# Optimization experiments

Hardware: AMD Instinct MI355X
Metric: run time of the kernel (lower is better)

Reference implementation:

```python
import jax, jax.numpy as jnp
import numpy as np

K = 3          # pooling factor (init k)
H_OUT = 8      # number of bilinear heads
H_DIM = 512    # hidden dim after pooling
BN_EPS = 1e-5
NEG_INF = -jnp.inf


def setup_inputs() -> dict:
    key = jax.random.key(0)
    ks = jax.random.split(key, 8)
    b, vn, qn, vd, qd = 16, 256, 256, 512, 768
    hk = H_DIM * K
    return {
        "v": jax.random.normal(ks[0], (b, vn, vd), jnp.float32),
        "q": jax.random.normal(ks[1], (b, qn, qd), jnp.float32),
        "Wv": jax.random.normal(ks[2], (hk, vd), jnp.float32) * 0.05,
        "bv": jax.random.normal(ks[3], (hk,), jnp.float32) * 0.05,
        "Wq": jax.random.normal(ks[4], (hk, qd), jnp.float32) * 0.05,
        "bq": jax.random.normal(ks[5], (hk,), jnp.float32) * 0.05,
        "h_mat": jax.random.normal(ks[6], (1, H_OUT, 1, hk), jnp.float32),
        "h_bias": jax.random.normal(ks[7], (1, H_OUT, 1, 1), jnp.float32),
        "bn_gamma": jnp.ones((H_DIM,), jnp.float32),
        "bn_beta": jnp.zeros((H_DIM,), jnp.float32),
    }


def _forward(v, q, Wv, bv, Wq, bq, h_mat, h_bias, bn_gamma, bn_beta):
    # FCNet (eval mode: dropout is identity; weight_norm folded into W)
    v_ = jax.nn.relu(jnp.einsum("bvd,kd->bvk", v, Wv) + bv)   # [b, vn, h_dim*k]
    q_ = jax.nn.relu(jnp.einsum("bqd,kd->bqk", q, Wq) + bq)   # [b, qn, h_dim*k]

    # Bilinear attention maps: [b, h_out, vn, qn]
    att = jnp.einsum("xhyk,bvk,bqk->bhvq", h_mat, v_, q_) + h_bias

    # v_mask / q_mask (all-zero token rows masked to -inf)
    v_zero = jnp.sum(jnp.abs(v), axis=2) == 0                  # [b, vn]
    q_zero = jnp.sum(jnp.abs(q), axis=2) == 0                  # [b, qn]
    att = jnp.where(v_zero[:, None, :, None], NEG_INF, att)
    att = jnp.where(q_zero[:, None, None, :], NEG_INF, att)

    # Fused per-head attention pooling, summed over heads (original Python loop)
    fused = jnp.einsum("bhvq,bqk->bhvk", att, q_)
    logits_k = jnp.einsum("bvk,bhvk->bk", v_, fused)           # [b, h_dim*k]

    # AvgPool1d(k, stride=k) * k  == sum over groups of k
    b = logits_k.shape[0]
    logits = logits_k.reshape(b, H_DIM, K).sum(axis=2)         # [b, h_dim]

    # BatchNorm1d (training-mode batch statistics, biased variance)
    mu = logits.mean(axis=0)
    var = logits.var(axis=0)
    logits = (logits - mu) * jax.lax.rsqrt(var + BN_EPS) * bn_gamma + bn_beta
    return logits, att


def reference(v, q, Wv, bv, Wq, bq, h_mat, h_bias, bn_gamma, bn_beta):
    return _forward(v, q, Wv, bv, Wq, bq, h_mat, h_bias, bn_gamma, bn_beta)
```

## Files before the change

### kernel.cpp

```cpp
#include <hip/hip_runtime.h>
#include <math.h>

#define BB    16
#define VN    256
#define QN    256
#define VD    512
#define QD    768
#define HK    1536
#define HDIM  512

typedef _Float16 half8 __attribute__((ext_vector_type(8)));
typedef _Float16 half4 __attribute__((ext_vector_type(4)));
typedef float f32x4 __attribute__((ext_vector_type(4)));

__global__ __launch_bounds__(256) void conv_mask2(
    const float* __restrict__ v, const float* __restrict__ q,
    _Float16* __restrict__ v16, _Float16* __restrict__ q16,
    float* __restrict__ vz, float* __restrict__ qz) {
    int which = blockIdx.y;
    const float* src = which ? q : v;
    _Float16* dst = which ? q16 : v16;
    float* outz = which ? qz : vz;
    int D = which ? QD : VD;
    int w = threadIdx.x >> 6, ln = threadIdx.x & 63;
    int row = blockIdx.x * 4 + w;
    const float* p = src + (size_t)row * D;
    _Float16* d = dst + (size_t)row * D;
    float s = 0.f;
    for (int c = ln * 4; c < D; c += 256) {
        float4 x = *(const float4*)(p + c);
        s += fabsf(x.x) + fabsf(x.y) + fabsf(x.z) + fabsf(x.w);
        half4 hh = {(_Float16)x.x, (_Float16)x.y, (_Float16)x.z, (_Float16)x.w};
        *(half4*)(d + c) = hh;
    }
    for (int off = 32; off > 0; off >>= 1) s += __shfl_down(s, off);
    if (ln == 0) outz[row] = (s == 0.f) ? 1.f : 0.f;
}

__global__ __launch_bounds__(256) void conv_w3(
    const float* __restrict__ Wv, _Float16* __restrict__ Wv16, int n4v,
    const float* __restrict__ Wq, _Float16* __restrict__ Wq16, int n4q,
    const float* __restrict__ hm, _Float16* __restrict__ hs16) {
    if (blockIdx.y == 2) {
        int k = blockIdx.x * 256 + threadIdx.x;
        if (k >= HK) return;
        float s = 0.f;
#pragma unroll
        for (int h = 0; h < 8; ++h) {
            float x = hm[h * HK + k];
            s += x;
            hs16[h * HK + k] = (_Float16)x;
        }
        hs16[8 * HK + k] = (_Float16)s;
        return;
    }
    const float* src = blockIdx.y ? Wq : Wv;
    _Float16* dst = blockIdx.y ? Wq16 : Wv16;
    int n4 = blockIdx.y ? n4q : n4v;
    int i = blockIdx.x * 256 + threadIdx.x;
    if (i < n4) {
        float4 x = ((const float4*)src)[i];
        half4 h = {(_Float16)x.x, (_Float16)x.y, (_Float16)x.z, (_Float16)x.w};
        ((half4*)dst)[i] = h;
    }
}

__global__ __launch_bounds__(128) void proj_lds(
    const _Float16* __restrict__ Ain, const _Float16* __restrict__ W16,
    const float* __restrict__ bias, _Float16* __restrict__ C16, int K) {
    __shared__ _Float16 As[64 * 64];
    __shared__ _Float16 Bs[64 * 64];
    int m0 = blockIdx.y * 64, n0 = blockIdx.x * 64;
    int t = threadIdx.x;
    int w = t >> 6, ln = t & 63, quad = ln >> 4, r16 = ln & 15;
    int arow = t >> 3, aseg = t & 7;
    int sg = aseg ^ (arow & 7);
    const _Float16* ApG = Ain + (size_t)(m0 + arow) * K + aseg * 8;
    const _Float16* BpG = W16 + (size_t)(n0 + arow) * K + aseg * 8;
    half8 ra[4], rb[4];
#pragma unroll
    for (int c = 0; c < 4; ++c) {
        ra[c] = *(const half8*)(ApG + (size_t)c * 16 * K);
        rb[c] = *(const half8*)(BpG + (size_t)c * 16 * K);
    }
    f32x4 acc[2][4] = {};
    for (int k0 = 0; k0 < K; k0 += 64) {
        __syncthreads();
#pragma unroll
        for (int c = 0; c < 4; ++c) {
            *(half8*)&As[(c * 16 + arow) * 64 + sg * 8] = ra[c];
            *(half8*)&Bs[(c * 16 + arow) * 64 + sg * 8] = rb[c];
        }
        __syncthreads();
        if (k0 + 64 < K) {
#pragma unroll
            for (int c = 0; c < 4; ++c) {
                ra[c] = *(const half8*)(ApG + (size_t)c * 16 * K + k0 + 64);
                rb[c] = *(const half8*)(BpG + (size_t)c * 16 * K + k0 + 64);
            }
        }
#pragma unroll
        for (int kc = 0; kc < 2; ++kc) {
            half8 af[2], bf[4];
#pragma unroll
            for (int fi = 0; fi < 2; ++fi) {
                int rl = w * 32 + fi * 16 + r16;
                af[fi] = *(const half8*)&As[rl * 64 + ((kc * 4 + quad) ^ (rl & 7)) * 8];
            }
#pragma unroll
            for (int fj = 0; fj < 4; ++fj) {
                int rl = fj * 16 + r16;
                bf[fj] = *(const half8*)&Bs[rl * 64 + ((kc * 4 + quad) ^ (rl & 7)) * 8];
            }
#pragma unroll
            for (int fi = 0; fi < 2; ++fi)
#pragma unroll
                for (int fj = 0; fj < 4; ++fj)
                    acc[fi][fj] = __builtin_amdgcn_mfma_f32_16x16x32_f16(
                        af[fi], bf[fj], acc[fi][fj], 0, 0, 0);
        }
    }
#pragma unroll
    for (int fi = 0; fi < 2; ++fi) {
#pragma unroll
        for (int r = 0; r < 4; ++r) {
            int m = m0 + w * 32 + fi * 16 + quad * 4 + r;
#pragma unroll
            for (int fj = 0; fj < 4; ++fj) {
                int n = n0 + fj * 16 + r16;
                float x = acc[fi][fj][r] + bias[n];
                C16[(size_t)m * HK + n] = (_Float16)fmaxf(x, 0.f);
            }
        }
    }
}

__global__ __launch_bounds__(256, 2) void att42(
    const _Float16* __restrict__ v16, const _Float16* __restrict__ q16,
    const _Float16* __restrict__ hs16, const float* __restrict__ hb,
    const float* __restrict__ vz, const float* __restrict__ qz,
    float* __restrict__ att_out, _Float16* __restrict__ A16) {
    __shared__ _Float16 As[64 * 64];
    __shared__ _Float16 Bs[32 * 64];
    __shared__ _Float16 Hl[8 * HK];
    int b = blockIdx.z;
    int i0 = blockIdx.y * 64, j0 = blockIdx.x * 32;
    int t = threadIdx.x;
    int w = t >> 6, ln = t & 63, quad = ln >> 4, r16 = ln & 15;
    int iw = w & 1, hg = w >> 1, h0 = hg * 4;
    int arow = t >> 2, as0 = t & 3;
    int brow = t >> 3, bs0 = t & 7;
    for (int u = t * 8; u < 8 * HK; u += 256 * 8)
        *(half8*)&Hl[u] = *(const half8*)(hs16 + u);
    const _Float16* ApG = v16 + (size_t)b * VN * HK + (size_t)(i0 + arow) * HK;
    const _Float16* BpG = q16 + (size_t)b * QN * HK + (size_t)(j0 + brow) * HK;
    half8 ra[2], rb;
    ra[0] = *(const half8*)(ApG + as0 * 8);
    ra[1] = *(const half8*)(ApG + as0 * 8 + 32);
    rb    = *(const half8*)(BpG + bs0 * 8);
    f32x4 acc[4][2][2] = {};
    for (int it = 0; it < 24; ++it) {
        __syncthreads();
        *(half8*)&As[arow * 64 + ((as0    ) ^ (arow & 7)) * 8] = ra[0];
        *(half8*)&As[arow * 64 + ((as0 + 4) ^ (arow & 7)) * 8] = ra[1];
        *(half8*)&Bs[brow * 64 + ((bs0    ) ^ (brow & 7)) * 8] = rb;
        __syncthreads();
        if (it + 1 < 24) {
            int kn = (it + 1) * 64;
            ra[0] = *(const half8*)(ApG + kn + as0 * 8);
            ra[1] = *(const half8*)(ApG + kn + as0 * 8 + 32);
            rb    = *(const half8*)(BpG + kn + bs0 * 8);
        }
        int kb = it * 64;
#pragma unroll
        for (int kc = 0; kc < 2; ++kc) {
            half8 af[2], bf[2];
#pragma unroll
            for (int fi = 0; fi < 2; ++fi) {
                int rl = iw * 32 + fi * 16 + r16;
                af[fi] = *(const half8*)&As[rl * 64 + ((kc * 4 + quad) ^ (rl & 7)) * 8];
            }
#pragma unroll
            for (int fj = 0; fj < 2; ++fj) {
                int rl = fj * 16 + r16;
                bf[fj] = *(const half8*)&Bs[rl * 64 + ((kc * 4 + quad) ^ (rl & 7)) * 8];
            }
#pragma unroll
            for (int hh = 0; hh < 4; ++hh) {
                half8 hmv = *(const half8*)&Hl[(h0 + hh) * HK + kb + (kc * 4 + quad) * 8];
#pragma unroll
                for (int fi = 0; fi < 2; ++fi) {
                    half8 am = af[fi] * hmv;
#pragma unroll
                    for (int fj = 0; fj < 2; ++fj)
                        acc[hh][fi][fj] = __builtin_amdgcn_mfma_f32_16x16x32_f16(
                            am, bf[fj], acc[hh][fi][fj], 0, 0, 0);
                }
            }
        }
    }
    float s[2][2][4];
#pragma unroll
    for (int fi = 0; fi < 2; ++fi)
#pragma unroll
        for (int fj = 0; fj < 2; ++fj)
#pragma unroll
            for (int r = 0; r < 4; ++r) {
                float ss = 0.f;
#pragma unroll
                for (int hh = 0; hh < 4; ++hh) ss += acc[hh][fi][fj][r];
                s[fi][fj][r] = ss;
            }
    float hbv[4];
#pragma unroll
    for (int hh = 0; hh < 4; ++hh) hbv[hh] = hb[h0 + hh];
    float hbsum = 0.f;
#pragma unroll
    for (int h = 0; h < 8; ++h) hbsum += hb[h];
    float qm[2];
#pragma unroll
    for (int fj = 0; fj < 2; ++fj) qm[fj] = qz[b * QN + j0 + fj * 16 + r16];
    float* outb = att_out + (size_t)b * 8 * VN * QN;
#pragma unroll
    for (int fi = 0; fi < 2; ++fi) {
#pragma unroll
        for (int r = 0; r < 4; ++r) {
            int i = i0 + iw * 32 + fi * 16 + quad * 4 + r;
            float vm = vz[b * VN + i];
#pragma unroll
            for (int fj = 0; fj < 2; ++fj) {
                int j = j0 + fj * 16 + r16;
                bool msk = (vm != 0.f) || (qm[fj] != 0.f);
#pragma unroll
                for (int hh = 0; hh < 4; ++hh) {
                    float x = acc[hh][fi][fj][r] + hbv[hh];
                    if (msk) x = -INFINITY;
                    outb[(size_t)(h0 + hh) * VN * QN + (size_t)i * QN + j] = x;
                }
            }
        }
    }
    __syncthreads();
    float* Red = (float*)As;
    if (hg) {
#pragma unroll
        for (int fi = 0; fi < 2; ++fi)
#pragma unroll
            for (int fj = 0; fj < 2; ++fj)
#pragma unroll
                for (int r = 0; r < 4; ++r)
                    Red[iw * 1024 + (fi * 16 + quad * 4 + r) * 32 + fj * 16 + r16] =
                        s[fi][fj][r];
    }
    __syncthreads();
    if (!hg) {
        _Float16* Ab = A16 + (size_t)b * VN * QN;
#pragma unroll
        for (int fi = 0; fi < 2; ++fi) {
#pragma unroll
            for (int r = 0; r < 4; ++r) {
                int i = i0 + iw * 32 + fi * 16 + quad * 4 + r;
                float vm = vz[b * VN + i];
#pragma unroll
                for (int fj = 0; fj < 2; ++fj) {
                    int j = j0 + fj * 16 + r16;
                    float tot = s[fi][fj][r] +
                                Red[iw * 1024 + (fi * 16 + quad * 4 + r) * 32 + fj * 16 + r16] +
                                hbsum;
                    if (vm != 0.f || qm[fj] != 0.f) tot = -INFINITY;
                    Ab[(size_t)i * QN + j] = (_Float16)tot;
                }
            }
        }
    }
}

__global__ __launch_bounds__(256) void transpose_q16(const _Float16* __restrict__ q16,
                                                     _Float16* __restrict__ q16t) {
    __shared__ _Float16 Ls[32][72];
    int b = blockIdx.z;
    int k0 = blockIdx.x * 64, j0 = blockIdx.y * 32;
    int t = threadIdx.x;
    const _Float16* src = q16 + (size_t)b * QN * HK;
    int tj = t >> 3, tk = (t & 7) * 8;
    half8 vv = *(const half8*)(src + (size_t)(j0 + tj) * HK + k0 + tk);
#pragma unroll
    for (int e = 0; e < 8; ++e) Ls[tj][tk + e] = vv[e];
    __syncthreads();
    int ok = t >> 2, oj = (t & 3) * 8;
    half8 ov;
#pragma unroll
    for (int e = 0; e < 8; ++e) ov[e] = Ls[oj + e][ok];
    *(half8*)(q16t + (size_t)b * HK * QN + (size_t)(k0 + ok) * QN + j0 + oj) = ov;
}

__global__ __launch_bounds__(256) void t_lk_mfma(
    const _Float16* __restrict__ A16, const _Float16* __restrict__ q16t,
    const _Float16* __restrict__ v16, float* __restrict__ lk) {
    __shared__ _Float16 As[256 * 32];
    __shared__ _Float16 Bs[64 * 32];
    __shared__ float red[16][64];
    int b = blockIdx.y;
    int k0 = blockIdx.x * 64;
    int t = threadIdx.x;
    int w = t >> 6, ln = t & 63, quad = ln >> 4, r16 = ln & 15;
    const _Float16* Ab = A16 + (size_t)b * VN * QN;
    const _Float16* Qt = q16t + (size_t)b * HK * QN + (size_t)k0 * QN;
    int ar = t >> 2, aseg = t & 3;
    f32x4 acc[4][4] = {};
    for (int j0 = 0; j0 < QN; j0 += 32) {
        half8 a0 = *(const half8*)(Ab + (size_t)(ar +   0) * QN + j0 + aseg * 8);
        half8 a1 = *(const half8*)(Ab + (size_t)(ar +  64) * QN + j0 + aseg * 8);
        half8 a2 = *(const half8*)(Ab + (size_t)(ar + 128) * QN + j0 + aseg * 8);
        half8 a3 = *(const half8*)(Ab + (size_t)(ar + 192) * QN + j0 + aseg * 8);
        half8 bv = *(const half8*)(Qt + (size_t)ar * QN + j0 + aseg * 8);
        __syncthreads();
        *(half8*)&As[(ar +   0) * 32 + aseg * 8] = a0;
        *(half8*)&As[(ar +  64) * 32 + aseg * 8] = a1;
        *(half8*)&As[(ar + 128) * 32 + aseg * 8] = a2;
        *(half8*)&As[(ar + 192) * 32 + aseg * 8] = a3;
        *(half8*)&Bs[ar * 32 + aseg * 8] = bv;
        __syncthreads();
        half8 af[4], bf[4];
#pragma unroll
        for (int fi = 0; fi < 4; ++fi)
            af[fi] = *(const half8*)&As[(w * 64 + fi * 16 + r16) * 32 + quad * 8];
#pragma unroll
        for (int fj = 0; fj < 4; ++fj)
            bf[fj] = *(const half8*)&Bs[(fj * 16 + r16) * 32 + quad * 8];
#pragma unroll
        for (int fi = 0; fi < 4; ++fi)
#pragma unroll
            for (int fj = 0; fj < 4; ++fj)
                acc[fi][fj] = __builtin_amdgcn_mfma_f32_16x16x32_f16(
                    af[fi], bf[fj], acc[fi][fj], 0, 0, 0);
    }
    const _Float16* Vb = v16 + (size_t)b * VN * HK;
    float part[4] = {0.f, 0.f, 0.f, 0.f};
#pragma unroll
    for (int fi = 0; fi < 4; ++fi) {
#pragma unroll
        for (int r = 0; r < 4; ++r) {
            int i = w * 64 + fi * 16 + quad * 4 + r;
#pragma unroll
            for (int fj = 0; fj < 4; ++fj) {
                float vv = (float)Vb[(size_t)i * HK + k0 + fj * 16 + r16];
                part[fj] += acc[fi][fj][r] * vv;
            }
        }
    }
#pragma unroll
    for (int fj = 0; fj < 4; ++fj)
        red[w * 4 + quad][fj * 16 + r16] = part[fj];
    __syncthreads();
    if (t < 64) {
        float s = 0.f;
#pragma unroll
        for (int g = 0; g < 16; ++g) s += red[g][t];
        lk[b * HK + k0 + t] = s;
    }
}

__global__ __launch_bounds__(256) void bn_kernel(
    const float* __restrict__ lk, const float* __restrict__ gamma,
    const float* __restrict__ beta, float* __restrict__ out) {
    int d = blockIdx.x * blockDim.x + threadIdx.x;
    if (d >= HDIM) return;
    float l[BB];
    float mu = 0.f;
#pragma unroll
    for (int b = 0; b < BB; ++b) {
        const float* p = lk + b * HK + 3 * d;
        float s = p[0] + p[1] + p[2];
        l[b] = s;
        mu += s;
    }
    mu *= (1.f / BB);
    float var = 0.f;
#pragma unroll
    for (int b = 0; b < BB; ++b) {
        float dd = l[b] - mu;
        var += dd * dd;
    }
    var *= (1.f / BB);
    float inv = rsqrtf(var + 1e-5f);
    float g = gamma[d], be = beta[d];
#pragma unroll
    for (int b = 0; b < BB; ++b)
        out[b * HDIM + d] = (l[b] - mu) * inv * g + be;
}

extern "C" void kernel_launch(void* const* d_in, const int* in_sizes, int n_in,
                              void* d_out, int out_size, void* d_ws, size_t ws_size,
                              hipStream_t stream) {
    const float* v  = (const float*)d_in[0];
    const float* q  = (const float*)d_in[1];
    const float* Wv = (const float*)d_in[2];
    const float* bv = (const float*)d_in[3];
    const float* Wq = (const float*)d_in[4];
    const float* bq = (const float*)d_in[5];
    const float* hm = (const float*)d_in[6];
    const float* hb = (const float*)d_in[7];
    const float* gamma = (const float*)d_in[8];
    const float* beta  = (const float*)d_in[9];

    float* out_logits = (float*)d_out;
    float* out_att    = out_logits + BB * HDIM;

    _Float16* h = (_Float16*)d_ws;
    _Float16* v16   = h;
    _Float16* q16   = v16 + (size_t)BB * VN * HK;
    _Float16* q16t  = q16 + (size_t)BB * QN * HK;
    _Float16* A16   = q16t + (size_t)BB * HK * QN;
    _Float16* v16in = A16 + (size_t)BB * VN * QN;
    _Float16* q16in = v16in + (size_t)BB * VN * VD;
    _Float16* Wv16  = q16in + (size_t)BB * QN * QD;
    _Float16* Wq16  = Wv16 + (size_t)HK * VD;
    _Float16* hs16  = Wq16 + (size_t)HK * QD;
    float* lk = (float*)(hs16 + 9 * HK + 8);
    float* vz = lk + BB * HK;
    float* qz = vz + BB * VN;

    conv_mask2<<<dim3(BB * VN / 4, 2), 256, 0, stream>>>(v, q, v16in, q16in, vz, qz);
    conv_w3<<<dim3((HK * QD / 4 + 255) / 256, 3), 256, 0, stream>>>(
        Wv, Wv16, HK * VD / 4, Wq, Wq16, HK * QD / 4, hm, hs16);

    proj_lds<<<dim3(HK / 64, BB * VN / 64), 128, 0, stream>>>(v16in, Wv16, bv, v16, VD);
    proj_lds<<<dim3(HK / 64, BB * QN / 64), 128, 0, stream>>>(q16in, Wq16, bq, q16, QD);

    att42<<<dim3(QN / 32, VN / 64, BB), 256, 0, stream>>>(
        v16, q16, hs16, hb, vz, qz, out_att, A16);

    transpose_q16<<<dim3(HK / 64, QN / 32, BB), 256, 0, stream>>>(q16, q16t);

    t_lk_mfma<<<dim3(HK / 64, BB), 256, 0, stream>>>(A16, q16t, v16, lk);

    bn_kernel<<<dim3((HDIM + 255) / 256), 256, 0, stream>>>(lk, gamma, beta, out_logits);
}
```

Before: 195.2 us.

## Double-buffer LDS tiles in attention kernel and swizzle block order

The attention-map kernel now keeps two LDS buffers for the v and q tiles and prefetches two K-steps ahead, so each iteration needs one barrier instead of two and global loads overlap with MFMA work. Global load mapping changes to 8 threads per row with full 64-element row segments. The grid becomes 1D with a swizzle that spreads consecutive blocks across batches and tiles, aimed at better L2/XCD locality. LDS use rises by one extra 6 KB tile set, which could affect occupancy at 2 blocks per CU.

```diff
diff --git a/kernel.cpp b/kernel.cpp
--- a/kernel.cpp
+++ b/kernel.cpp
@@ -135,41 +135,54 @@
     }
 }
 
-__global__ __launch_bounds__(256, 2) void att42(
+__global__ __launch_bounds__(256, 2) void att_db(
     const _Float16* __restrict__ v16, const _Float16* __restrict__ q16,
     const _Float16* __restrict__ hs16, const float* __restrict__ hb,
     const float* __restrict__ vz, const float* __restrict__ qz,
     float* __restrict__ att_out, _Float16* __restrict__ A16) {
-    __shared__ _Float16 As[64 * 64];
-    __shared__ _Float16 Bs[32 * 64];
+    __shared__ _Float16 As[2][64 * 64];
+    __shared__ _Float16 Bs[2][32 * 64];
     __shared__ _Float16 Hl[8 * HK];
-    int b = blockIdx.z;
-    int i0 = blockIdx.y * 64, j0 = blockIdx.x * 32;
+    int lin = blockIdx.x;
+    int swz = ((lin & 7) << 6) | (lin >> 3);
+    int jb = swz & 7, ib = (swz >> 3) & 3, b = swz >> 5;
+    int i0 = ib * 64, j0 = jb * 32;
     int t = threadIdx.x;
     int w = t >> 6, ln = t & 63, quad = ln >> 4, r16 = ln & 15;
     int iw = w & 1, hg = w >> 1, h0 = hg * 4;
-    int arow = t >> 2, as0 = t & 3;
-    int brow = t >> 3, bs0 = t & 7;
+    int arow = t >> 3, aseg = t & 7;
+    int sg = (aseg ^ (arow & 7)) * 8;
     for (int u = t * 8; u < 8 * HK; u += 256 * 8)
         *(half8*)&Hl[u] = *(const half8*)(hs16 + u);
-    const _Float16* ApG = v16 + (size_t)b * VN * HK + (size_t)(i0 + arow) * HK;
-    const _Float16* BpG = q16 + (size_t)b * QN * HK + (size_t)(j0 + brow) * HK;
+    const _Float16* ApG = v16 + (size_t)b * VN * HK + (size_t)(i0 + arow) * HK + aseg * 8;
+    const _Float16* BpG = q16 + (size_t)b * QN * HK + (size_t)(j0 + arow) * HK + aseg * 8;
     half8 ra[2], rb;
-    ra[0] = *(const half8*)(ApG + as0 * 8);
-    ra[1] = *(const half8*)(ApG + as0 * 8 + 32);
-    rb    = *(const half8*)(BpG + bs0 * 8);
+    ra[0] = *(const half8*)(ApG);
+    ra[1] = *(const half8*)(ApG + (size_t)32 * HK);
+    rb    = *(const half8*)(BpG);
+    *(half8*)&As[0][arow * 64 + sg] = ra[0];
+    *(half8*)&As[0][(arow + 32) * 64 + sg] = ra[1];
+    *(half8*)&Bs[0][arow * 64 + sg] = rb;
+    ra[0] = *(const half8*)(ApG + 64);
+    ra[1] = *(const half8*)(ApG + (size_t)32 * HK + 64);
+    rb    = *(const half8*)(BpG + 64);
     f32x4 acc[4][2][2] = {};
     for (int it = 0; it < 24; ++it) {
         __syncthreads();
-        *(half8*)&As[arow * 64 + ((as0    ) ^ (arow & 7)) * 8] = ra[0];
-        *(half8*)&As[arow * 64 + ((as0 + 4) ^ (arow & 7)) * 8] = ra[1];
-        *(half8*)&Bs[brow * 64 + ((bs0    ) ^ (brow & 7)) * 8] = rb;
-        __syncthreads();
+        int cur = it & 1;
+        const _Float16* Ac = As[cur];
+        const _Float16* Bc = Bs[cur];
         if (it + 1 < 24) {
-            int kn = (it + 1) * 64;
-            ra[0] = *(const half8*)(ApG + kn + as0 * 8);
-            ra[1] = *(const half8*)(ApG + kn + as0 * 8 + 32);
-            rb    = *(const half8*)(BpG + kn + bs0 * 8);
+            int nxt = cur ^ 1;
+            *(half8*)&As[nxt][arow * 64 + sg] = ra[0];
+            *(half8*)&As[nxt][(arow + 32) * 64 + sg] = ra[1];
+            *(half8*)&Bs[nxt][arow * 64 + sg] = rb;
+        }
+        if (it + 2 < 24) {
+            int kn = (it + 2) * 64;
+            ra[0] = *(const half8*)(ApG + kn);
+            ra[1] = *(const half8*)(ApG + (size_t)32 * HK + kn);
+            rb    = *(const half8*)(BpG + kn);
         }
         int kb = it * 64;
 #pragma unroll
@@ -178,12 +191,12 @@
 #pragma unroll
             for (int fi = 0; fi < 2; ++fi) {
                 int rl = iw * 32 + fi * 16 + r16;
-                af[fi] = *(const half8*)&As[rl * 64 + ((kc * 4 + quad) ^ (rl & 7)) * 8];
+                af[fi] = *(const half8*)&Ac[rl * 64 + ((kc * 4 + quad) ^ (rl & 7)) * 8];
             }
 #pragma unroll
             for (int fj = 0; fj < 2; ++fj) {
                 int rl = fj * 16 + r16;
-                bf[fj] = *(const half8*)&Bs[rl * 64 + ((kc * 4 + quad) ^ (rl & 7)) * 8];
+                bf[fj] = *(const half8*)&Bc[rl * 64 + ((kc * 4 + quad) ^ (rl & 7)) * 8];
             }
 #pragma unroll
             for (int hh = 0; hh < 4; ++hh) {
@@ -241,7 +254,7 @@
         }
     }
     __syncthreads();
-    float* Red = (float*)As;
+    float* Red = (float*)&As[0][0];
     if (hg) {
 #pragma unroll
         for (int fi = 0; fi < 2; ++fi)
@@ -428,7 +441,7 @@
     proj_lds<<<dim3(HK / 64, BB * VN / 64), 128, 0, stream>>>(v16in, Wv16, bv, v16, VD);
     proj_lds<<<dim3(HK / 64, BB * QN / 64), 128, 0, stream>>>(q16in, Wq16, bq, q16, QD);
 
-    att42<<<dim3(QN / 32, VN / 64, BB), 256, 0, stream>>>(
+    att_db<<<dim3(512), 256, 0, stream>>>(
         v16, q16, hs16, hb, vz, qz, out_att, A16);
 
     transpose_q16<<<dim3(HK / 64, QN / 32, BB), 256, 0, stream>>>(q16, q16t);
```

New measurement: 189.6 us. -2.9%, faster.

## Replace LDS-staged attention kernel with direct global-load MFMA kernel and swizzled grid

Applied to the files above, without the earlier changes.

Rewrites the bilinear attention kernel so each wave loads its A, B and h_mat fragments straight from global memory (relying on L1/L2), dropping the shared-memory staging, the per-iteration barriers and the 24KB h_mat LDS copy. Blocks shrink to 128 threads covering a 32x32 tile with two head groups, launched as a flat 1D grid with a swizzle that places neighbouring tiles on different blocks. It aims to cut LDS traffic and synchronisation and raise occupancy. The cost is redundant global/cache loads, since v and q rows are no longer shared across waves, and smaller tiles mean more total fragment reads.

```diff
diff --git a/kernel.cpp b/kernel.cpp
--- a/kernel.cpp
+++ b/kernel.cpp
@@ -135,62 +135,43 @@
     }
 }
 
-__global__ __launch_bounds__(256, 2) void att42(
+__global__ __launch_bounds__(128, 3) void att_nolds(
     const _Float16* __restrict__ v16, const _Float16* __restrict__ q16,
     const _Float16* __restrict__ hs16, const float* __restrict__ hb,
     const float* __restrict__ vz, const float* __restrict__ qz,
     float* __restrict__ att_out, _Float16* __restrict__ A16) {
-    __shared__ _Float16 As[64 * 64];
-    __shared__ _Float16 Bs[32 * 64];
-    __shared__ _Float16 Hl[8 * HK];
-    int b = blockIdx.z;
-    int i0 = blockIdx.y * 64, j0 = blockIdx.x * 32;
+    __shared__ float Red[32 * 32];
+    int lin = blockIdx.x;
+    int swz = ((lin & 7) << 7) | (lin >> 3);
+    int jb = swz & 7, ib = (swz >> 3) & 7, b = swz >> 6;
+    int i0 = ib * 32, j0 = jb * 32;
     int t = threadIdx.x;
-    int w = t >> 6, ln = t & 63, quad = ln >> 4, r16 = ln & 15;
-    int iw = w & 1, hg = w >> 1, h0 = hg * 4;
-    int arow = t >> 2, as0 = t & 3;
-    int brow = t >> 3, bs0 = t & 7;
-    for (int u = t * 8; u < 8 * HK; u += 256 * 8)
-        *(half8*)&Hl[u] = *(const half8*)(hs16 + u);
-    const _Float16* ApG = v16 + (size_t)b * VN * HK + (size_t)(i0 + arow) * HK;
-    const _Float16* BpG = q16 + (size_t)b * QN * HK + (size_t)(j0 + brow) * HK;
-    half8 ra[2], rb;
-    ra[0] = *(const half8*)(ApG + as0 * 8);
-    ra[1] = *(const half8*)(ApG + as0 * 8 + 32);
-    rb    = *(const half8*)(BpG + bs0 * 8);
+    int hg = t >> 6, ln = t & 63, quad = ln >> 4, r16 = ln & 15;
+    int h0 = hg * 4;
+    const _Float16* Av = v16 + (size_t)b * VN * HK + (size_t)(i0 + r16) * HK + quad * 8;
+    const _Float16* Bq = q16 + (size_t)b * QN * HK + (size_t)(j0 + r16) * HK + quad * 8;
+    const _Float16* Hm = hs16 + (size_t)h0 * HK + quad * 8;
     f32x4 acc[4][2][2] = {};
     for (int it = 0; it < 24; ++it) {
-        __syncthreads();
-        *(half8*)&As[arow * 64 + ((as0    ) ^ (arow & 7)) * 8] = ra[0];
-        *(half8*)&As[arow * 64 + ((as0 + 4) ^ (arow & 7)) * 8] = ra[1];
-        *(half8*)&Bs[brow * 64 + ((bs0    ) ^ (brow & 7)) * 8] = rb;
-        __syncthreads();
-        if (it + 1 < 24) {
-            int kn = (it + 1) * 64;
-            ra[0] = *(const half8*)(ApG + kn + as0 * 8);
-            ra[1] = *(const half8*)(ApG + kn + as0 * 8 + 32);
-            rb    = *(const half8*)(BpG + kn + bs0 * 8);
-        }
         int kb = it * 64;
 #pragma unroll
         for (int kc = 0; kc < 2; ++kc) {
-            half8 af[2], bf[2];
-#pragma unroll
-            for (int fi = 0; fi < 2; ++fi) {
-                int rl = iw * 32 + fi * 16 + r16;
-                af[fi] = *(const half8*)&As[rl * 64 + ((kc * 4 + quad) ^ (rl & 7)) * 8];
-            }
-#pragma unroll
-            for (int fj = 0; fj < 2; ++fj) {
-                int rl = fj * 16 + r16;
-                bf[fj] = *(const half8*)&Bs[rl * 64 + ((kc * 4 + quad) ^ (rl & 7)) * 8];
-            }
+            int ko = kb + kc * 32;
+            half8 af[2], bf[2], hmv[4];
+#pragma unroll
+            for (int fi = 0; fi < 2; ++fi)
+                af[fi] = *(const half8*)(Av + (size_t)fi * 16 * HK + ko);
+#pragma unroll
+            for (int fj = 0; fj < 2; ++fj)
+                bf[fj] = *(const half8*)(Bq + (size_t)fj * 16 * HK + ko);
+#pragma unroll
+            for (int hh = 0; hh < 4; ++hh)
+                hmv[hh] = *(const half8*)(Hm + (size_t)hh * HK + ko);
 #pragma unroll
             for (int hh = 0; hh < 4; ++hh) {
-                half8 hmv = *(const half8*)&Hl[(h0 + hh) * HK + kb + (kc * 4 + quad) * 8];
 #pragma unroll
                 for (int fi = 0; fi < 2; ++fi) {
-                    half8 am = af[fi] * hmv;
+                    half8 am = af[fi] * hmv[hh];
 #pragma unroll
                     for (int fj = 0; fj < 2; ++fj)
                         acc[hh][fi][fj] = __builtin_amdgcn_mfma_f32_16x16x32_f16(
@@ -225,7 +206,7 @@
     for (int fi = 0; fi < 2; ++fi) {
 #pragma unroll
         for (int r = 0; r < 4; ++r) {
-            int i = i0 + iw * 32 + fi * 16 + quad * 4 + r;
+            int i = i0 + fi * 16 + quad * 4 + r;
             float vm = vz[b * VN + i];
 #pragma unroll
             for (int fj = 0; fj < 2; ++fj) {
@@ -240,8 +221,6 @@
             }
         }
     }
-    __syncthreads();
-    float* Red = (float*)As;
     if (hg) {
 #pragma unroll
         for (int fi = 0; fi < 2; ++fi)
@@ -249,8 +228,7 @@
             for (int fj = 0; fj < 2; ++fj)
 #pragma unroll
                 for (int r = 0; r < 4; ++r)
-                    Red[iw * 1024 + (fi * 16 + quad * 4 + r) * 32 + fj * 16 + r16] =
-                        s[fi][fj][r];
+                    Red[(fi * 16 + quad * 4 + r) * 32 + fj * 16 + r16] = s[fi][fj][r];
     }
     __syncthreads();
     if (!hg) {
@@ -259,14 +237,13 @@
         for (int fi = 0; fi < 2; ++fi) {
 #pragma unroll
             for (int r = 0; r < 4; ++r) {
-                int i = i0 + iw * 32 + fi * 16 + quad * 4 + r;
+                int i = i0 + fi * 16 + quad * 4 + r;
                 float vm = vz[b * VN + i];
 #pragma unroll
                 for (int fj = 0; fj < 2; ++fj) {
                     int j = j0 + fj * 16 + r16;
                     float tot = s[fi][fj][r] +
-                                Red[iw * 1024 + (fi * 16 + quad * 4 + r) * 32 + fj * 16 + r16] +
-                                hbsum;
+                                Red[(fi * 16 + quad * 4 + r) * 32 + fj * 16 + r16] + hbsum;
                     if (vm != 0.f || qm[fj] != 0.f) tot = -INFINITY;
                     Ab[(size_t)i * QN + j] = (_Float16)tot;
                 }
@@ -428,7 +405,7 @@
     proj_lds<<<dim3(HK / 64, BB * VN / 64), 128, 0, stream>>>(v16in, Wv16, bv, v16, VD);
     proj_lds<<<dim3(HK / 64, BB * QN / 64), 128, 0, stream>>>(q16in, Wq16, bq, q16, QD);
 
-    att42<<<dim3(QN / 32, VN / 64, BB), 256, 0, stream>>>(
+    att_nolds<<<dim3(1024), 128, 0, stream>>>(
         v16, q16, hs16, hb, vz, qz, out_att, A16);
 
     transpose_q16<<<dim3(HK / 64, QN / 32, BB), 256, 0, stream>>>(q16, q16t);
```

Measured after the change: 217.4 us. 1.11x slower.
